# Optimization experiments

Hardware: AMD Instinct MI355X
Metric: run time of the kernel (lower is better)

The kernel has to match this reference:

```python
import jax, jax.numpy as jnp
import numpy as np

B, N_ATOMS = 64, 32        # graphs, atoms per graph (equal-sized graphs)
HID = 600                  # hidden_channels == num_filters
NG = 50                    # num_gaussians
NL = 6                     # num_interactions
CUTOFF = 10.0
BOX = 8.0                  # box edge (A); max pair dist ~13.8 so cutoff masks some pairs
ZMAX = 100                 # PyG SchNet atomic-number embedding size
LOG2 = 0.6931471805599453


def ssp(x):
    # ShiftedSoftplus: softplus(x) - log(2)
    return jax.nn.softplus(x) - LOG2


def setup_inputs() -> dict:
    key = jax.random.key(0)
    ks = jax.random.split(key, 12)
    N = B * N_ATOMS
    z = jax.random.randint(ks[0], (N,), 0, ZMAX, dtype=jnp.int32)
    pos = jax.random.uniform(ks[1], (N, 3), dtype=jnp.float32) * BOX
    batch = jnp.repeat(jnp.arange(B, dtype=jnp.int32), N_ATOMS)

    def w(k, shape, fan_in):
        return jax.random.normal(k, shape, dtype=jnp.float32) / np.float32(np.sqrt(fan_in))

    return {
        "z": z, "pos": pos, "batch": batch,
        "emb": w(ks[2], (ZMAX, HID), 1.0),
        # stacked per-interaction params (scanned over NL layers)
        "mlp_w1": w(ks[3], (NL, NG, HID), NG),   "mlp_b1": jnp.zeros((NL, HID), jnp.float32),
        "mlp_w2": w(ks[4], (NL, HID, HID), HID), "mlp_b2": jnp.zeros((NL, HID), jnp.float32),
        "lin1_w": w(ks[5], (NL, HID, HID), HID),  # CFConv lin1 has no bias
        "lin2_w": w(ks[6], (NL, HID, HID), HID), "lin2_b": jnp.zeros((NL, HID), jnp.float32),
        "lin_w": w(ks[7], (NL, HID, HID), HID),  "lin_b": jnp.zeros((NL, HID), jnp.float32),
        "pool_w": w(ks[8], (HID, HID), HID),     "pool_b": jnp.zeros((HID,), jnp.float32),
    }


def _forward(z, pos, batch, emb, mlp_w1, mlp_b1, mlp_w2, mlp_b2,
             lin1_w, lin2_w, lin2_b, lin_w, lin_b, pool_w, pool_b):
    # equal-sized graphs -> block-dense radius graph per graph
    p = pos.reshape(B, N_ATOMS, 3)
    diff = p[:, :, None, :] - p[:, None, :, :]           # [B,n,n,3]
    sq = jnp.sum(diff * diff, axis=-1)                   # [B,n,n]
    eye = jnp.eye(N_ATOMS, dtype=bool)
    mask = (sq <= CUTOFF * CUTOFF) & (~eye)              # radius_graph, no self loops
    d = jnp.sqrt(jnp.where(sq > 0, sq, 1.0))             # safe sqrt (diag masked out)

    # GaussianSmearing(0, cutoff, NG)
    offset = jnp.linspace(0.0, CUTOFF, NG).astype(pos.dtype)
    coeff = -0.5 / (offset[1] - offset[0]) ** 2
    rbf = jnp.exp(coeff * (d[..., None] - offset) ** 2)  # [B,n,n,NG]
    # cosine cutoff, zeroed outside the radius graph
    cosw = (0.5 * (jnp.cos(d * jnp.pi / CUTOFF) + 1.0)) * mask  # [B,n,n]

    h = emb[z].reshape(B, N_ATOMS, HID)                  # atom embedding

    def interaction(h, prm):
        w1, b1, w2, b2, l1w, l2w, l2b, lw, lb = prm
        # CFConv filter network on edge attrs: Linear -> ssp -> Linear, then cosine cutoff
        W = ssp(rbf @ w1 + b1) @ w2 + b2                 # [B,n,n,HID]
        W = W * cosw[..., None]
        xj = h @ l1w                                     # lin1 (no bias)
        m = jnp.einsum('bijf,bjf->bif', W, xj)           # message + scatter-add over neighbors
        v = ssp(m @ l2w + l2b)                           # lin2 then ShiftedSoftplus
        v = v @ lw + lb                                  # interaction output linear
        return h + v, None                               # residual update

    prms = (mlp_w1, mlp_b1, mlp_w2, mlp_b2, lin1_w, lin2_w, lin2_b, lin_w, lin_b)
    h, _ = jax.lax.scan(interaction, h, prms)

    pooled = h.mean(axis=1)                              # per-graph mean pooling [B,HID]
    return pooled @ pool_w + pool_b                      # pool_proj


def reference(z, pos, batch, emb, mlp_w1, mlp_b1, mlp_w2, mlp_b2,
              lin1_w, lin2_w, lin2_b, lin_w, lin_b, pool_w, pool_b):
    return _forward(z, pos, batch, emb, mlp_w1, mlp_b1, mlp_w2, mlp_b2,
                    lin1_w, lin2_w, lin2_b, lin_w, lin_b, pool_w, pool_b)
```

## Files before the change

### kernel.cpp

```cpp
#include <hip/hip_runtime.h>
#include <hip/hip_bf16.h>
#include <math.h>

#define BB 64
#define NA 32
#define NTOT 2048
#define HID 600
#define KP  640
#define NG 50
#define NL 6
#define NEDGE 65536
#define TK 608

typedef __attribute__((ext_vector_type(8))) short short8;
typedef __attribute__((ext_vector_type(4))) float f32x4;

typedef __attribute__((address_space(1))) const void gvoid_t;
typedef __attribute__((address_space(3))) void lvoid_t;

__device__ __forceinline__ float sspf(float x) {
    return (x > 15.f) ? (x - 0.69314718056f)
                      : __logf(0.5f + 0.5f * __expf(x));
}
__device__ __forceinline__ unsigned short f2bf(float x) {
    union { float f; unsigned u; } v; v.f = x;
    unsigned r = v.u + 0x7FFF + ((v.u >> 16) & 1);
    return (unsigned short)(r >> 16);
}

__global__ void prep_edges(const float* __restrict__ pos,
                           unsigned short* __restrict__ rbf_bf,
                           float* __restrict__ cw) {
    int e = blockIdx.x * blockDim.x + threadIdx.x;
    if (e >= NEDGE) return;
    int b  = e >> 10;
    int ij = e & 1023;
    int i = ij >> 5, j = ij & 31;
    int ai = b*NA + i, aj = b*NA + j;
    float dx = pos[ai*3+0] - pos[aj*3+0];
    float dy = pos[ai*3+1] - pos[aj*3+1];
    float dz = pos[ai*3+2] - pos[aj*3+2];
    float sq = dx*dx + dy*dy + dz*dz;
    float d  = sqrtf(sq > 0.f ? sq : 1.f);
    float msk = ((sq <= 100.f) && (i != j)) ? 1.f : 0.f;
    cw[e] = 0.5f * (cosf(d * 0.31415926535f) + 1.f) * msk;
    const float step  = 10.f / 49.f;
    const float coeff = -0.5f / (step*step);
    #pragma unroll
    for (int g8 = 0; g8 < 8; g8++) {
        union { unsigned short us[8]; uint4 v; } u;
        #pragma unroll
        for (int q = 0; q < 8; q++) {
            int g = g8*8 + q;
            float t = d - step * (float)g;
            float val = (g < NG) ? __expf(coeff * t * t) : 0.f;
            u.us[q] = f2bf(val);
        }
        *(uint4*)(rbf_bf + (size_t)e*64 + g8*8) = u.v;
    }
}

__global__ void transpose_w(const float* __restrict__ src,
                            unsigned short* __restrict__ dst) {
    __shared__ float tile[64][65];
    int kb = blockIdx.x*64, fb = blockIdx.y*64, l = blockIdx.z;
    const float* s = src + (size_t)l*HID*HID;
    unsigned short* d = dst + (size_t)l*KP*KP;
    int tid = threadIdx.x;
    #pragma unroll 4
    for (int i = 0; i < 16; i++) {
        int idx = tid + 256*i;
        int r = idx >> 6, c = idx & 63;
        float v = 0.f;
        if (kb + r < HID && fb + c < HID) v = s[(size_t)(kb+r)*HID + fb + c];
        tile[r][c] = v;
    }
    __syncthreads();
    #pragma unroll 4
    for (int i = 0; i < 16; i++) {
        int idx = tid + 256*i;
        int fr = idx >> 6, kc = idx & 63;
        d[(size_t)(fb+fr)*KP + kb + kc] = f2bf(tile[kc][fr]);
    }
}

__global__ void transpose_w1(const float* __restrict__ w1,
                             unsigned short* __restrict__ w1t) {
    int idx = blockIdx.x;
    int l = idx / KP, fr = idx - l*KP;
    int k = threadIdx.x;
    float v = (fr < HID && k < NG) ? w1[(size_t)l*NG*HID + (size_t)k*HID + fr] : 0.f;
    w1t[((size_t)l*KP + fr)*64 + k] = f2bf(v);
}

__global__ void gather_h(const int* __restrict__ z, const float* __restrict__ emb,
                         float* __restrict__ h, unsigned short* __restrict__ h_bf) {
    int n = blockIdx.x;
    int zi = z[n];
    for (int f = threadIdx.x; f < KP; f += blockDim.x) {
        float v = (f < HID) ? emb[(size_t)zi*HID + f] : 0.f;
        if (f < HID) h[(size_t)n*HID + f] = v;
        h_bf[(size_t)n*KP + f] = f2bf(v);
    }
}

__global__ __launch_bounds__(256, 2) void edge_mfma(
    const unsigned short* __restrict__ rbf_bf, const float* __restrict__ cw,
    const float* __restrict__ xj,
    const unsigned short* __restrict__ w1t, const float* __restrict__ b1,
    const unsigned short* __restrict__ w2t, const float* __restrict__ b2,
    unsigned short* __restrict__ m_bf)
{
    __shared__ __align__(16) char t_smem[64*1216];
    __shared__ float cw_s[64];

    const int tid  = threadIdx.x;
    const int wave = tid >> 6, lane = tid & 63;
    const int cl = lane & 15, gr = lane >> 4;
    const int i0 = blockIdx.x * 2;
    const int ebase = i0 * NA;
    const int jbase = i0 & ~(NA-1);

    if (tid < 64) cw_s[tid] = cw[ebase + tid];

    {
        short8 a1[4][2];
        #pragma unroll
        for (int fr = 0; fr < 4; fr++)
            #pragma unroll
            for (int ks = 0; ks < 2; ks++)
                a1[fr][ks] = *(const short8*)(rbf_bf + (size_t)(ebase + fr*16 + cl)*64 + ks*32 + gr*8);

        for (int p = 0; p < 10; p++) {
            int ft = wave + 4*p;
            if (ft < 38) {
                f32x4 acc[4] = {};
                #pragma unroll
                for (int ks = 0; ks < 2; ks++) {
                    short8 bfr = *(const short8*)(w1t + (size_t)(ft*16 + cl)*64 + ks*32 + gr*8);
                    #pragma unroll
                    for (int fr = 0; fr < 4; fr++)
                        acc[fr] = __builtin_amdgcn_mfma_f32_16x16x32_bf16(a1[fr][ks], bfr, acc[fr], 0, 0, 0);
                }
                int f = ft*16 + cl;
                float b1v = (f < HID) ? b1[f] : 0.f;
                #pragma unroll
                for (int fr = 0; fr < 4; fr++)
                    #pragma unroll
                    for (int r = 0; r < 4; r++) {
                        int row = fr*16 + gr*4 + r;
                        float tv = sspf(acc[fr][r] + b1v);
                        int byt = row*1216 + f*2;
                        *(unsigned short*)(t_smem + (byt ^ ((row & 7) << 4))) = f2bf(tv);
                    }
            }
        }
    }
    __syncthreads();

    #define LOAD_S(Sb, kk)                                                        \
        _Pragma("unroll")                                                         \
        for (int s = 0; s < 5; s++)                                               \
            Sb[s] = *(const short8*)(pBg + (size_t)s*16*KP + (kk));

    #define MFMA_STEP(Sb, kk)                                                     \
        {                                                                         \
            short8 a_[4];                                                         \
            _Pragma("unroll")                                                     \
            for (int fr = 0; fr < 4; fr++) {                                      \
                int row = fr*16 + cl;                                             \
                a_[fr] = *(const short8*)(t_smem +                                \
                          ((row*1216 + (kk)*2 + gr*16) ^ ((row & 7) << 4)));      \
            }                                                                     \
            _Pragma("unroll")                                                     \
            for (int s = 0; s < 5; s++)                                           \
                _Pragma("unroll")                                                 \
                for (int fr = 0; fr < 4; fr++)                                    \
                    acc[s][fr] = __builtin_amdgcn_mfma_f32_16x16x32_bf16(         \
                        a_[fr], Sb[s], acc[s][fr], 0, 0, 0);                      \
        }

    for (int grp = 0; grp < 2; grp++) {
        const int ft0 = wave*10 + grp*5;
        const unsigned short* pBg = w2t + (size_t)(ft0*16 + cl)*KP + gr*8;
        f32x4 acc[5][4] = {};
        short8 S0[5], S1[5], S2[5];

        LOAD_S(S0, 0)
        LOAD_S(S1, 32)

        #pragma unroll 1
        for (int it = 0; it < 6; it++) {
            const int k0 = it*96;
            LOAD_S(S2, k0+64)
            MFMA_STEP(S0, k0)
            LOAD_S(S0, k0+96)
            MFMA_STEP(S1, k0+32)
            LOAD_S(S1, k0+128)
            MFMA_STEP(S2, k0+64)
        }
        MFMA_STEP(S0, 576)

        #pragma unroll
        for (int s = 0; s < 5; s++) {
            int f = (ft0 + s)*16 + cl;
            if (f < HID) {
                float b2v = b2[f];
                float s0 = 0.f, s1 = 0.f;
                #pragma unroll
                for (int r = 0; r < 4; r++) {
                    float xa = xj[(size_t)(jbase + gr*4 + r)*HID + f];
                    float xb = xj[(size_t)(jbase + 16 + gr*4 + r)*HID + f];
                    s0 += cw_s[gr*4 + r]      * (acc[s][0][r] + b2v) * xa;
                    s0 += cw_s[16 + gr*4 + r] * (acc[s][1][r] + b2v) * xb;
                    s1 += cw_s[32 + gr*4 + r] * (acc[s][2][r] + b2v) * xa;
                    s1 += cw_s[48 + gr*4 + r] * (acc[s][3][r] + b2v) * xb;
                }
                s0 += __shfl_xor(s0, 16); s0 += __shfl_xor(s0, 32);
                s1 += __shfl_xor(s1, 16); s1 += __shfl_xor(s1, 32);
                if (gr == 0) {
                    m_bf[(size_t)i0*KP + f]     = f2bf(s0);
                    m_bf[(size_t)(i0+1)*KP + f] = f2bf(s1);
                }
            } else if (gr == 0 && f < KP) {
                m_bf[(size_t)i0*KP + f]     = 0;
                m_bf[(size_t)(i0+1)*KP + f] = 0;
            }
        }
    }
    #undef LOAD_S
    #undef MFMA_STEP
}

template<int ACT, int RES>
__global__ __launch_bounds__(256, 4) void gemm_bf(
    const unsigned short* __restrict__ A,
    const unsigned short* __restrict__ Wt,
    const float* __restrict__ bias,
    const float* __restrict__ res,
    float* __restrict__ Cf,
    unsigned short* __restrict__ Cb,
    int M)
{
    __shared__ __align__(16) unsigned short As[2][64*64];
    __shared__ __align__(16) unsigned short Bs[2][64*64];
    const int tid = threadIdx.x;
    const int wave = tid >> 6, lane = tid & 63;
    const int cl = lane & 15, gr = lane >> 4;
    const int row0 = blockIdx.x * 64, f0 = blockIdx.y * 64;

    const int r0 = tid >> 3, sc = tid & 7;
    const size_t swz = 8*(sc ^ (r0 & 7));
    const unsigned short* gA = A  + (size_t)(row0 + r0)*KP + swz;
    const unsigned short* gB = Wt + (size_t)(f0   + r0)*KP + swz;

    f32x4 acc[4] = {};

    {
        __builtin_amdgcn_global_load_lds((gvoid_t*)(gA),         (lvoid_t*)&As[0][wave*512],        16, 0, 0);
        __builtin_amdgcn_global_load_lds((gvoid_t*)(gA + 32*KP), (lvoid_t*)&As[0][2048 + wave*512], 16, 0, 0);
        __builtin_amdgcn_global_load_lds((gvoid_t*)(gB),         (lvoid_t*)&Bs[0][wave*512],        16, 0, 0);
        __builtin_amdgcn_global_load_lds((gvoid_t*)(gB + 32*KP), (lvoid_t*)&Bs[0][2048 + wave*512], 16, 0, 0);
    }

    int buf = 0;
    const int rb_ = wave*16 + cl;
    const int bxor = (rb_ & 7) << 4;
    for (int t = 0; t < 10; t++) {
        __syncthreads();
        if (t < 9) {
            int k0 = (t+1)*64;
            __builtin_amdgcn_global_load_lds((gvoid_t*)(gA + k0),         (lvoid_t*)&As[buf^1][wave*512],        16, 0, 0);
            __builtin_amdgcn_global_load_lds((gvoid_t*)(gA + k0 + 32*KP), (lvoid_t*)&As[buf^1][2048 + wave*512], 16, 0, 0);
            __builtin_amdgcn_global_load_lds((gvoid_t*)(gB + k0),         (lvoid_t*)&Bs[buf^1][wave*512],        16, 0, 0);
            __builtin_amdgcn_global_load_lds((gvoid_t*)(gB + k0 + 32*KP), (lvoid_t*)&Bs[buf^1][2048 + wave*512], 16, 0, 0);
        }
        const char* pa = (const char*)As[buf];
        const char* pb = (const char*)Bs[buf];
        #pragma unroll
        for (int ks = 0; ks < 2; ks++) {
            short8 b = *(const short8*)(pb + (rb_*128 + ((ks*64 + gr*16) ^ bxor)));
            #pragma unroll
            for (int fr = 0; fr < 4; fr++) {
                int ra_ = fr*16 + cl;
                short8 a = *(const short8*)(pa + (ra_*128 + ((ks*64 + gr*16) ^ ((ra_ & 7) << 4))));
                acc[fr] = __builtin_amdgcn_mfma_f32_16x16x32_bf16(a, b, acc[fr], 0, 0, 0);
            }
        }
        buf ^= 1;
    }

    const int fcol = f0 + wave*16 + cl;
    #pragma unroll
    for (int fr = 0; fr < 4; fr++) {
        #pragma unroll
        for (int r = 0; r < 4; r++) {
            int row = row0 + fr*16 + gr*4 + r;
            float x = acc[fr][r];
            if (fcol < HID) {
                if (bias) x += bias[fcol];
                if (ACT) x = sspf(x);
                if (RES) x += res[(size_t)row*HID + fcol];
                if (Cf) Cf[(size_t)row*HID + fcol] = x;
                if (Cb) Cb[(size_t)row*KP + fcol] = f2bf(x);
            } else if (Cb) {
                Cb[(size_t)row*KP + fcol] = 0;
            }
        }
    }
}

template<int ACT, int RES>
__global__ __launch_bounds__(256) void gemm64(
    const float* __restrict__ A, const float* __restrict__ W,
    const float* __restrict__ bias, const float* __restrict__ res,
    float* __restrict__ C, int M, int K, int Nn)
{
    __shared__ float Asm[64][17];
    __shared__ float Wsm[16][64];
    const int tid = threadIdx.x;
    const int rb = blockIdx.x * 64, cb = blockIdx.y * 64;
    const int tx = tid & 15, ty = tid >> 4;

    float accv[4][4] = {};
    const int ar = tid >> 2;
    const int ak = (tid & 3) * 4;
    const int wk = tid >> 4;
    const int wc = (tid & 15) * 4;

    for (int k0 = 0; k0 < K; k0 += 16) {
        float4 av = make_float4(0.f,0.f,0.f,0.f);
        if (k0 + ak < K)
            av = *(const float4*)&A[(size_t)(rb+ar)*K + k0 + ak];
        float4 wv = make_float4(0.f,0.f,0.f,0.f);
        if (k0 + wk < K && cb + wc < Nn)
            wv = *(const float4*)&W[(size_t)(k0+wk)*Nn + cb + wc];
        __syncthreads();
        Asm[ar][ak+0]=av.x; Asm[ar][ak+1]=av.y; Asm[ar][ak+2]=av.z; Asm[ar][ak+3]=av.w;
        *(float4*)&Wsm[wk][wc] = wv;
        __syncthreads();
        #pragma unroll
        for (int kk = 0; kk < 16; kk++) {
            float4 wrow = *(const float4*)&Wsm[kk][tx*4];
            float wr[4] = {wrow.x, wrow.y, wrow.z, wrow.w};
            float aa[4] = {Asm[ty*4+0][kk], Asm[ty*4+1][kk],
                           Asm[ty*4+2][kk], Asm[ty*4+3][kk]};
            #pragma unroll
            for (int u = 0; u < 4; u++)
                #pragma unroll
                for (int v = 0; v < 4; v++)
                    accv[u][v] = fmaf(aa[u], wr[v], accv[u][v]);
        }
    }
    #pragma unroll
    for (int u = 0; u < 4; u++) {
        int r = rb + ty*4 + u;
        #pragma unroll
        for (int v = 0; v < 4; v++) {
            int c = cb + tx*4 + v;
            if (c < Nn) {
                float x = accv[u][v];
                if (bias) x += bias[c];
                if (ACT == 1) x = sspf(x);
                if (RES) x += res[(size_t)r*Nn + c];
                C[(size_t)r*Nn + c] = x;
            }
        }
    }
}

__global__ void pool_mean(const float* __restrict__ h, float* __restrict__ pooled) {
    int b = blockIdx.x;
    for (int f = threadIdx.x; f < HID; f += blockDim.x) {
        float s = 0.f;
        #pragma unroll
        for (int i = 0; i < NA; i++) s += h[(size_t)(b*NA+i)*HID + f];
        pooled[(size_t)b*HID + f] = s * (1.f/NA);
    }
}

extern "C" void kernel_launch(void* const* d_in, const int* in_sizes, int n_in,
                              void* d_out, int out_size, void* d_ws, size_t ws_size,
                              hipStream_t stream)
{
    const int*   z    = (const int*)  d_in[0];
    const float* pos  = (const float*)d_in[1];
    const float* emb  = (const float*)d_in[3];
    const float* mw1  = (const float*)d_in[4];
    const float* mb1  = (const float*)d_in[5];
    const float* mw2  = (const float*)d_in[6];
    const float* mb2  = (const float*)d_in[7];
    const float* l1w  = (const float*)d_in[8];
    const float* l2w  = (const float*)d_in[9];
    const float* l2b  = (const float*)d_in[10];
    const float* lw   = (const float*)d_in[11];
    const float* lb   = (const float*)d_in[12];
    const float* pw   = (const float*)d_in[13];
    const float* pb   = (const float*)d_in[14];

    char* p = (char*)d_ws;
    unsigned short* rbf_bf = (unsigned short*)p; p += (size_t)NEDGE*64*2;
    float*          cwb    = (float*)p;          p += (size_t)NEDGE*4;
    unsigned short* w1t    = (unsigned short*)p; p += (size_t)NL*KP*64*2;
    unsigned short* wt2    = (unsigned short*)p; p += (size_t)NL*KP*KP*2;
    unsigned short* wtl1   = (unsigned short*)p; p += (size_t)NL*KP*KP*2;
    unsigned short* wtl2   = (unsigned short*)p; p += (size_t)NL*KP*KP*2;
    unsigned short* wtl    = (unsigned short*)p; p += (size_t)NL*KP*KP*2;
    float*          h      = (float*)p;          p += (size_t)NTOT*HID*4;
    unsigned short* h_bf   = (unsigned short*)p; p += (size_t)NTOT*KP*2;
    float*          xj     = (float*)p;          p += (size_t)NTOT*HID*4;
    unsigned short* m_bf   = (unsigned short*)p; p += (size_t)NTOT*KP*2;
    unsigned short* v1_bf  = (unsigned short*)p; p += (size_t)NTOT*KP*2;
    float*          pooled = (float*)p;          p += (size_t)BB*HID*4;

    prep_edges<<<NEDGE/256, 256, 0, stream>>>(pos, rbf_bf, cwb);
    dim3 tg(10, 10, NL);
    transpose_w<<<tg, 256, 0, stream>>>(mw2, wt2);
    transpose_w<<<tg, 256, 0, stream>>>(l1w, wtl1);
    transpose_w<<<tg, 256, 0, stream>>>(l2w, wtl2);
    transpose_w<<<tg, 256, 0, stream>>>(lw,  wtl);
    transpose_w1<<<NL*KP, 64, 0, stream>>>(mw1, w1t);
    gather_h<<<NTOT, 256, 0, stream>>>(z, emb, h, h_bf);

    dim3 gg(NTOT/64, KP/64);
    for (int l = 0; l < NL; l++) {
        const float* b1l  = mb1 + (size_t)l*HID;
        const float* b2l  = mb2 + (size_t)l*HID;
        const float* l2bl = l2b + (size_t)l*HID;
        const float* lbl  = lb  + (size_t)l*HID;

        gemm_bf<0,0><<<gg, 256, 0, stream>>>(h_bf, wtl1 + (size_t)l*KP*KP,
                                             nullptr, nullptr, xj, nullptr, NTOT);
        edge_mfma<<<NTOT/2, 256, 0, stream>>>(rbf_bf, cwb, xj,
                                              w1t + (size_t)l*KP*64, b1l,
                                              wt2 + (size_t)l*KP*KP, b2l, m_bf);
        gemm_bf<1,0><<<gg, 256, 0, stream>>>(m_bf, wtl2 + (size_t)l*KP*KP,
                                             l2bl, nullptr, nullptr, v1_bf, NTOT);
        gemm_bf<0,1><<<gg, 256, 0, stream>>>(v1_bf, wtl + (size_t)l*KP*KP,
                                             lbl, h, h, h_bf, NTOT);
    }

    pool_mean<<<BB, 256, 0, stream>>>(h, pooled);
    gemm64<0,0><<<dim3(1, 10), 256, 0, stream>>>(pooled, pw, pb, nullptr,
                                                 (float*)d_out, BB, HID, HID);
}
```

Baseline: 1.279 ms.

## Pack filter weights into MFMA fragment order and transpose xj for coalesced loads

Adds a pack_w2 kernel that stores the filter-network second-layer weights in a tiled layout matching the MFMA B-fragment order. Each lane's loads in the edge kernel become contiguous 1 KB-strided chunks instead of rows strided by KP. The lin1 GEMM now writes xj transposed (feature-major), so the edge epilogue reads four neighbours with one float4 instead of four strided scalar loads. The LDS swizzle is also changed and the A addresses are precomputed. The cost is uncoalesced transposed stores in the lin1 GEMM epilogue, plus a changed bank pattern that could conflict.

```diff
diff --git a/kernel.cpp b/kernel.cpp
--- a/kernel.cpp
+++ b/kernel.cpp
@@ -11,6 +11,7 @@
 #define NL 6
 #define NEDGE 65536
 #define TK 608
+#define W2G_L (8*19*5*512)
 
 typedef __attribute__((ext_vector_type(8))) short short8;
 typedef __attribute__((ext_vector_type(4))) float f32x4;
@@ -84,6 +85,24 @@
     }
 }
 
+__global__ void pack_w2(const float* __restrict__ src,
+                        unsigned short* __restrict__ dst) {
+    int t = blockIdx.x, g = blockIdx.y, l = blockIdx.z;
+    #pragma unroll
+    for (int i = 0; i < 10; i++) {
+        int flat = i*256 + threadIdx.x;
+        int cl = flat & 15;
+        int e  = (flat >> 4) & 7;
+        int gr = (flat >> 7) & 3;
+        int s  = flat >> 9;
+        int f = g*80 + s*16 + cl;
+        int k = t*32 + gr*8 + e;
+        float v = (f < HID && k < HID) ? src[(size_t)l*HID*HID + (size_t)k*HID + f] : 0.f;
+        size_t di = (size_t)l*W2G_L + (((size_t)(g*19 + t)*5 + s)*512) + cl*32 + gr*8 + e;
+        dst[di] = f2bf(v);
+    }
+}
+
 __global__ void transpose_w1(const float* __restrict__ w1,
                              unsigned short* __restrict__ w1t) {
     int idx = blockIdx.x;
@@ -106,9 +125,9 @@
 
 __global__ __launch_bounds__(256, 2) void edge_mfma(
     const unsigned short* __restrict__ rbf_bf, const float* __restrict__ cw,
-    const float* __restrict__ xj,
+    const float* __restrict__ xjT,
     const unsigned short* __restrict__ w1t, const float* __restrict__ b1,
-    const unsigned short* __restrict__ w2t, const float* __restrict__ b2,
+    const unsigned short* __restrict__ w2g, const float* __restrict__ b2,
     unsigned short* __restrict__ m_bf)
 {
     __shared__ __align__(16) char t_smem[64*1216];
@@ -151,70 +170,79 @@
                         int row = fr*16 + gr*4 + r;
                         float tv = sspf(acc[fr][r] + b1v);
                         int byt = row*1216 + f*2;
-                        *(unsigned short*)(t_smem + (byt ^ ((row & 7) << 4))) = f2bf(tv);
+                        *(unsigned short*)(t_smem + (byt ^ (((row >> 2) & 3) << 4))) = f2bf(tv);
                     }
             }
         }
     }
     __syncthreads();
 
-    #define LOAD_S(Sb, kk)                                                        \
-        _Pragma("unroll")                                                         \
-        for (int s = 0; s < 5; s++)                                               \
-            Sb[s] = *(const short8*)(pBg + (size_t)s*16*KP + (kk));
-
-    #define MFMA_STEP(Sb, kk)                                                     \
-        {                                                                         \
-            short8 a_[4];                                                         \
-            _Pragma("unroll")                                                     \
-            for (int fr = 0; fr < 4; fr++) {                                      \
-                int row = fr*16 + cl;                                             \
-                a_[fr] = *(const short8*)(t_smem +                                \
-                          ((row*1216 + (kk)*2 + gr*16) ^ ((row & 7) << 4)));      \
-            }                                                                     \
-            _Pragma("unroll")                                                     \
-            for (int s = 0; s < 5; s++)                                           \
-                _Pragma("unroll")                                                 \
-                for (int fr = 0; fr < 4; fr++)                                    \
-                    acc[s][fr] = __builtin_amdgcn_mfma_f32_16x16x32_bf16(         \
-                        a_[fr], Sb[s], acc[s][fr], 0, 0, 0);                      \
+    int abase[4];
+    #pragma unroll
+    for (int fr = 0; fr < 4; fr++) {
+        int row = fr*16 + cl;
+        abase[fr] = (row*1216 + gr*16) ^ (((row >> 2) & 3) << 4);
+    }
+
+    #define LOADB(Sb, OFF)                                                       \
+        _Pragma("unroll")                                                        \
+        for (int s = 0; s < 5; s++)                                              \
+            Sb[s] = *(const short8*)(pB + (OFF) + s*1024 - 2048);
+
+    #define ASTEP(Sb, KO)                                                        \
+        {                                                                        \
+            short8 a_[4];                                                        \
+            _Pragma("unroll")                                                    \
+            for (int fr = 0; fr < 4; fr++)                                       \
+                a_[fr] = *(const short8*)(pa + abase[fr] + (KO));                 \
+            _Pragma("unroll")                                                    \
+            for (int s = 0; s < 5; s++)                                          \
+                _Pragma("unroll")                                                \
+                for (int fr = 0; fr < 4; fr++)                                   \
+                    acc[s][fr] = __builtin_amdgcn_mfma_f32_16x16x32_bf16(        \
+                        a_[fr], Sb[s], acc[s][fr], 0, 0, 0);                     \
         }
 
     for (int grp = 0; grp < 2; grp++) {
-        const int ft0 = wave*10 + grp*5;
-        const unsigned short* pBg = w2t + (size_t)(ft0*16 + cl)*KP + gr*8;
+        const int g = wave*2 + grp;
+        const char* pB = (const char*)(w2g + (size_t)g*19*5*512) + cl*64 + gr*16 + 2048;
+        const char* pa = t_smem;
         f32x4 acc[5][4] = {};
         short8 S0[5], S1[5], S2[5];
 
-        LOAD_S(S0, 0)
-        LOAD_S(S1, 32)
+        LOADB(S0, 0)
+        LOADB(S1, 5120)
 
         #pragma unroll 1
         for (int it = 0; it < 6; it++) {
-            const int k0 = it*96;
-            LOAD_S(S2, k0+64)
-            MFMA_STEP(S0, k0)
-            LOAD_S(S0, k0+96)
-            MFMA_STEP(S1, k0+32)
-            LOAD_S(S1, k0+128)
-            MFMA_STEP(S2, k0+64)
-        }
-        MFMA_STEP(S0, 576)
+            LOADB(S2, 10240)
+            ASTEP(S0, 0)
+            LOADB(S0, 15360)
+            ASTEP(S1, 64)
+            LOADB(S1, 20480)
+            ASTEP(S2, 128)
+            pB += 15360;
+            pa += 192;
+        }
+        ASTEP(S0, 0)
 
         #pragma unroll
         for (int s = 0; s < 5; s++) {
-            int f = (ft0 + s)*16 + cl;
+            int f = (g*5 + s)*16 + cl;
             if (f < HID) {
                 float b2v = b2[f];
+                const float* xcol = xjT + (size_t)f*NTOT + jbase;
+                float4 xa = *(const float4*)(xcol + gr*4);
+                float4 xb = *(const float4*)(xcol + 16 + gr*4);
+                const float* xaf = (const float*)&xa;
+                const float* xbf = (const float*)&xb;
                 float s0 = 0.f, s1 = 0.f;
                 #pragma unroll
                 for (int r = 0; r < 4; r++) {
-                    float xa = xj[(size_t)(jbase + gr*4 + r)*HID + f];
-                    float xb = xj[(size_t)(jbase + 16 + gr*4 + r)*HID + f];
-                    s0 += cw_s[gr*4 + r]      * (acc[s][0][r] + b2v) * xa;
-                    s0 += cw_s[16 + gr*4 + r] * (acc[s][1][r] + b2v) * xb;
-                    s1 += cw_s[32 + gr*4 + r] * (acc[s][2][r] + b2v) * xa;
-                    s1 += cw_s[48 + gr*4 + r] * (acc[s][3][r] + b2v) * xb;
+                    s0 += cw_s[gr*4 + r]      * (acc[s][0][r] + b2v) * xaf[r];
+                    s0 += cw_s[16 + gr*4 + r] * (acc[s][1][r] + b2v) * xbf[r];
+                    s1 += cw_s[32 + gr*4 + r] * (acc[s][2][r] + b2v) * xaf[r];
+                    s1 += cw_s[48 + gr*4 + r] * (acc[s][3][r] + b2v) * xbf[r];
                 }
                 s0 += __shfl_xor(s0, 16); s0 += __shfl_xor(s0, 32);
                 s1 += __shfl_xor(s1, 16); s1 += __shfl_xor(s1, 32);
@@ -228,8 +256,8 @@
             }
         }
     }
-    #undef LOAD_S
-    #undef MFMA_STEP
+    #undef LOADB
+    #undef ASTEP
 }
 
 template<int ACT, int RES>
@@ -239,6 +267,7 @@
     const float* __restrict__ bias,
     const float* __restrict__ res,
     float* __restrict__ Cf,
+    float* __restrict__ CfT,
     unsigned short* __restrict__ Cb,
     int M)
 {
@@ -301,8 +330,9 @@
                 if (bias) x += bias[fcol];
                 if (ACT) x = sspf(x);
                 if (RES) x += res[(size_t)row*HID + fcol];
-                if (Cf) Cf[(size_t)row*HID + fcol] = x;
-                if (Cb) Cb[(size_t)row*KP + fcol] = f2bf(x);
+                if (Cf)  Cf[(size_t)row*HID + fcol] = x;
+                if (CfT) CfT[(size_t)fcol*NTOT + row] = x;
+                if (Cb)  Cb[(size_t)row*KP + fcol] = f2bf(x);
             } else if (Cb) {
                 Cb[(size_t)row*KP + fcol] = 0;
             }
@@ -402,20 +432,20 @@
     unsigned short* rbf_bf = (unsigned short*)p; p += (size_t)NEDGE*64*2;
     float*          cwb    = (float*)p;          p += (size_t)NEDGE*4;
     unsigned short* w1t    = (unsigned short*)p; p += (size_t)NL*KP*64*2;
-    unsigned short* wt2    = (unsigned short*)p; p += (size_t)NL*KP*KP*2;
+    unsigned short* w2g    = (unsigned short*)p; p += (size_t)NL*W2G_L*2;
     unsigned short* wtl1   = (unsigned short*)p; p += (size_t)NL*KP*KP*2;
     unsigned short* wtl2   = (unsigned short*)p; p += (size_t)NL*KP*KP*2;
     unsigned short* wtl    = (unsigned short*)p; p += (size_t)NL*KP*KP*2;
     float*          h      = (float*)p;          p += (size_t)NTOT*HID*4;
     unsigned short* h_bf   = (unsigned short*)p; p += (size_t)NTOT*KP*2;
-    float*          xj     = (float*)p;          p += (size_t)NTOT*HID*4;
+    float*          xjT    = (float*)p;          p += (size_t)KP*NTOT*4;
     unsigned short* m_bf   = (unsigned short*)p; p += (size_t)NTOT*KP*2;
     unsigned short* v1_bf  = (unsigned short*)p; p += (size_t)NTOT*KP*2;
     float*          pooled = (float*)p;          p += (size_t)BB*HID*4;
 
     prep_edges<<<NEDGE/256, 256, 0, stream>>>(pos, rbf_bf, cwb);
+    pack_w2<<<dim3(19, 8, NL), 256, 0, stream>>>(mw2, w2g);
     dim3 tg(10, 10, NL);
-    transpose_w<<<tg, 256, 0, stream>>>(mw2, wt2);
     transpose_w<<<tg, 256, 0, stream>>>(l1w, wtl1);
     transpose_w<<<tg, 256, 0, stream>>>(l2w, wtl2);
     transpose_w<<<tg, 256, 0, stream>>>(lw,  wtl);
@@ -430,14 +460,14 @@
         const float* lbl  = lb  + (size_t)l*HID;
 
         gemm_bf<0,0><<<gg, 256, 0, stream>>>(h_bf, wtl1 + (size_t)l*KP*KP,
-                                             nullptr, nullptr, xj, nullptr, NTOT);
-        edge_mfma<<<NTOT/2, 256, 0, stream>>>(rbf_bf, cwb, xj,
+                                             nullptr, nullptr, nullptr, xjT, nullptr, NTOT);
+        edge_mfma<<<NTOT/2, 256, 0, stream>>>(rbf_bf, cwb, xjT,
                                               w1t + (size_t)l*KP*64, b1l,
-                                              wt2 + (size_t)l*KP*KP, b2l, m_bf);
+                                              w2g + (size_t)l*W2G_L, b2l, m_bf);
         gemm_bf<1,0><<<gg, 256, 0, stream>>>(m_bf, wtl2 + (size_t)l*KP*KP,
-                                             l2bl, nullptr, nullptr, v1_bf, NTOT);
+                                             l2bl, nullptr, nullptr, nullptr, v1_bf, NTOT);
         gemm_bf<0,1><<<gg, 256, 0, stream>>>(v1_bf, wtl + (size_t)l*KP*KP,
-                                             lbl, h, h, h_bf, NTOT);
+                                             lbl, h, h, nullptr, h_bf, NTOT);
     }
 
     pool_mean<<<BB, 256, 0, stream>>>(h, pooled);
```

Measured after the change: 1.074 ms. 16.0% less time.
